# Performance work log

Measured on AMD Instinct MI355X. Metric: run time of the kernel, lower is better.

Reference implementation:

```python
import jax, jax.numpy as jnp
import numpy as np

B, C, H, W = 8, 64, 96, 320
K = 50
HEAD = 256
CLS = 3
CIN3 = C + 2 + CLS  # feat + 2 coord maps + one-hot class


def _conv(x, w, b, pad):
    y = jax.lax.conv_general_dilated(x, w, (1, 1), [(pad, pad), (pad, pad)],
                                     dimension_numbers=('NCHW', 'OIHW', 'NCHW'))
    return y + b[None, :, None, None]


def _head2(x, w1, b1, w2, b2):
    # Conv3x3 -> ReLU -> Conv1x1 (heatmap / offset_2d / size_2d heads)
    return _conv(jax.nn.relu(_conv(x, w1, b1, 1)), w2, b2, 0)


def _head3(x, w1, b1, g, be, m, v, w2, b2):
    # Conv3x3 -> BN(eval) -> ReLU -> AdaptiveAvgPool2d(1) -> Conv1x1, returns [N, cout]
    y = _conv(x, w1, b1, 1)
    y = (y - m[None, :, None, None]) * (g * jax.lax.rsqrt(v + 1e-5))[None, :, None, None] + be[None, :, None, None]
    y = jax.nn.relu(y).mean((2, 3))
    return y @ w2.reshape(w2.shape[0], -1).T + b2


def _nms(heat):
    hmax = jax.lax.reduce_window(heat, -jnp.inf, jax.lax.max, (1, 1, 3, 3), (1, 1, 1, 1), 'SAME')
    return jnp.where(hmax == heat, heat, 0.0)


def _roi_align(feat, boxes, out=7, sr=2):
    # torchvision roi_align semantics (spatial_scale=1, aligned=False, sampling_ratio=2);
    # boxes are treated as constants w.r.t. gradients (as in torchvision).
    boxes = jax.lax.stop_gradient(boxes)
    b = boxes[:, 0].astype(jnp.int32)
    x1, y1, x2, y2 = boxes[:, 1], boxes[:, 2], boxes[:, 3], boxes[:, 4]
    bw = jnp.maximum(x2 - x1, 1.0) / out
    bh = jnp.maximum(y2 - y1, 1.0) / out
    g = (jnp.arange(out * sr, dtype=feat.dtype) + 0.5) / sr  # sample positions in bin units
    ys = y1[:, None] + g[None, :] * bh[:, None]  # [N, S]
    xs = x1[:, None] + g[None, :] * bw[:, None]
    Hf, Wf = feat.shape[2], feat.shape[3]
    def prep(c, dim):
        valid = (c >= -1.0) & (c <= dim)
        c = jnp.clip(c, 0.0, dim - 1.0)
        i0 = jnp.floor(c).astype(jnp.int32)
        i1 = jnp.minimum(i0 + 1, dim - 1)
        return i0, i1, c - i0, valid
    y0, y1i, fy, vy = prep(ys, Hf)
    x0, x1i, fx, vx = prep(xs, Wf)
    bb = b[:, None, None]
    def gather(yi, xi):
        return feat[bb, :, yi[:, :, None], xi[:, None, :]]  # [N, S, S, C]
    w00 = ((1 - fy)[:, :, None] * (1 - fx)[:, None, :])[..., None]
    w01 = ((1 - fy)[:, :, None] * fx[:, None, :])[..., None]
    w10 = (fy[:, :, None] * (1 - fx)[:, None, :])[..., None]
    w11 = (fy[:, :, None] * fx[:, None, :])[..., None]
    val = gather(y0, x0) * w00 + gather(y0, x1i) * w01 + gather(y1i, x0) * w10 + gather(y1i, x1i) * w11
    val = val * (vy[:, :, None] & vx[:, None, :])[..., None].astype(feat.dtype)
    N = boxes.shape[0]
    val = val.reshape(N, out, sr, out, sr, -1).mean((2, 4))  # avg over sampling grid
    return val.transpose(0, 3, 1, 2)  # [N, C, 7, 7]


def _project2rect(calib, p):
    f_u, f_v = calib[:, 0, 0], calib[:, 1, 1]
    c_u, c_v = calib[:, 0, 2], calib[:, 1, 2]
    b_x = calib[:, 0, 3] / -f_u
    b_y = calib[:, 1, 3] / -f_v
    x = (p[:, 0] - c_u) * p[:, 2] / f_u + b_x
    y = (p[:, 1] - c_v) * p[:, 2] / f_v + b_y
    return jnp.stack([x, y, p[:, 2]], -1)


def reference(feat, coord_ranges, calibs, mean_size, hm_w1, hm_b1, hm_w2, hm_b2, o2_w1, o2_b1, o2_w2, o2_b2, s2_w1, s2_b1, s2_w2, s2_b2, dep_w1, dep_b1, dep_g, dep_be, dep_m, dep_v, dep_w2, dep_b2, o3_w1, o3_b1, o3_g, o3_be, o3_m, o3_v, o3_w2, o3_b2, s3_w1, s3_b1, s3_g, s3_be, s3_m, s3_v, s3_w2, s3_b2, hd_w1, hd_b1, hd_g, hd_be, hd_m, hd_v, hd_w2, hd_b2):
    # dense 2D heads
    heatmap = _head2(feat, hm_w1, hm_b1, hm_w2, hm_b2)        # [B,1,H,W]
    offset_2d = _head2(feat, o2_w1, o2_b1, o2_w2, o2_b2)      # [B,2,H,W]
    size_2d = _head2(feat, s2_w1, s2_b1, s2_w2, s2_b2)        # [B,2,H,W]
    # test-mode: NMS + topK (single-class heatmap -> cls ids all 0)
    heat = _nms(jnp.clip(jax.nn.sigmoid(heatmap), 1e-4, 1.0 - 1e-4))
    _, inds = jax.lax.top_k(heat.reshape(B, -1), K)           # [B,K]
    cls_flat = jnp.zeros((B * K,), jnp.int32)
    # box2d maps in feature coords
    xg = jnp.arange(W, dtype=feat.dtype)
    yg = jnp.arange(H, dtype=feat.dtype)
    coord_map = jnp.stack([jnp.broadcast_to(xg[None, :], (H, W)), jnp.broadcast_to(yg[:, None], (H, W))], 0)
    centre = coord_map[None] + offset_2d
    box2d = jnp.concatenate([centre - size_2d / 2, centre + size_2d / 2], 1)  # [B,4,H,W]
    bidx = jnp.broadcast_to(jnp.arange(B, dtype=feat.dtype)[:, None, None, None], (B, 1, H, W))
    bm = jnp.concatenate([bidx, box2d], 1).reshape(B, 5, H * W)
    boxes = jnp.take_along_axis(bm, inds[:, None, :], 2).transpose(0, 2, 1).reshape(B * K, 5)
    roi = _roi_align(feat, boxes)                             # [N,64,7,7]
    bsel = boxes[:, 0].astype(jnp.int32)
    cr = coord_ranges[bsel]
    sx = cr[:, 1, 0] - cr[:, 0, 0]
    sy = cr[:, 1, 1] - cr[:, 0, 1]
    boxes_r = jnp.stack([boxes[:, 0],
                         boxes[:, 1] / W * sx + cr[:, 0, 0],
                         boxes[:, 2] / H * sy + cr[:, 0, 1],
                         boxes[:, 3] / W * sx + cr[:, 0, 0],
                         boxes[:, 4] / H * sy + cr[:, 0, 1]], -1)
    roi_calibs = calibs[bsel]
    ones = jnp.ones((B * K, 1), feat.dtype)
    p1 = _project2rect(roi_calibs, jnp.concatenate([boxes_r[:, 1:3], ones], -1))[:, :2]
    p2 = _project2rect(roi_calibs, jnp.concatenate([boxes_r[:, 3:5], ones], -1))[:, :2]
    cam = jnp.concatenate([p1, p2], -1)                       # [N,4]
    t = jnp.arange(7, dtype=feat.dtype) / 6.0
    xs7 = cam[:, 0:1] + t[None, :] * (cam[:, 2:3] - cam[:, 0:1])
    ys7 = cam[:, 1:2] + t[None, :] * (cam[:, 3:4] - cam[:, 1:2])
    cmx = jnp.broadcast_to(xs7[:, None, None, :], (B * K, 1, 7, 7))
    cmy = jnp.broadcast_to(ys7[:, None, :, None], (B * K, 1, 7, 7))
    hots = jax.nn.one_hot(cls_flat, CLS, dtype=feat.dtype)
    roi_full = jnp.concatenate([roi, cmx, cmy, jnp.broadcast_to(hots[:, :, None, None], (B * K, CLS, 7, 7))], 1)
    h2d = jnp.maximum(boxes_r[:, 4] - boxes_r[:, 2], 1.0)
    s3 = _head3(roi_full, s3_w1, s3_b1, s3_g, s3_be, s3_m, s3_v, s3_w2, s3_b2)  # [N,4]
    h3d_log_std = s3[:, 3:4]
    size3d_offset = s3[:, :3]
    size_3d = mean_size[cls_flat] + size3d_offset
    f_u = roi_calibs[:, 0, 0]
    depth_geo = size_3d[:, 0] / h2d * f_u
    dno = _head3(roi_full, dep_w1, dep_b1, dep_g, dep_be, dep_m, dep_v, dep_w2, dep_b2)  # [N,2]
    geo_log_std = (h3d_log_std[:, 0] + 2.0 * (jnp.log(f_u) - jnp.log(h2d)))[:, None]
    net_log_std = jax.nn.logsumexp(jnp.concatenate([dno[:, 1:2], geo_log_std], -1), -1, keepdims=True)
    depth = jnp.concatenate([1.0 / (jax.nn.sigmoid(dno[:, 0:1]) + 1e-6) - 1.0 + depth_geo[:, None], net_log_std], -1)
    heading = _head3(roi_full, hd_w1, hd_b1, hd_g, hd_be, hd_m, hd_v, hd_w2, hd_b2)
    offset_3d = _head3(roi_full, o3_w1, o3_b1, o3_g, o3_be, o3_m, o3_v, o3_w2, o3_b2)
    return (heatmap, offset_2d, size_2d, heading, depth, offset_3d, size3d_offset, h3d_log_std)


def setup_inputs() -> dict:
    keys = iter(jax.random.split(jax.random.key(0), 40))
    def rn(shape, s=0.05):
        return jax.random.normal(next(keys), shape, jnp.float32) * s
    d = {}
    d['feat'] = jax.random.normal(next(keys), (B, C, H, W), jnp.float32)
    d['coord_ranges'] = jnp.tile(jnp.array([[0.0, 0.0], [1280.0, 384.0]], jnp.float32)[None], (B, 1, 1))
    d['calibs'] = jnp.tile(jnp.array([[720.0, 0.0, 640.0, 0.04], [0.0, 720.0, 190.0, 0.01], [0.0, 0.0, 1.0, 0.003]], jnp.float32)[None], (B, 1, 1))
    d['mean_size'] = jnp.array([[1.52, 1.63, 3.88], [1.73, 0.67, 0.88], [1.77, 0.60, 1.76]], jnp.float32)
    for pfx, cout in [('hm', 1), ('o2', 2), ('s2', 2)]:
        d[pfx + '_w1'] = rn((HEAD, C, 3, 3))
        d[pfx + '_b1'] = jnp.zeros((HEAD,), jnp.float32)
        d[pfx + '_w2'] = rn((cout, HEAD, 1, 1))
        d[pfx + '_b2'] = jnp.full((cout,), -2.19, jnp.float32) if pfx == 'hm' else jnp.zeros((cout,), jnp.float32)
    for pfx, cout in [('dep', 2), ('o3', 2), ('s3', 4), ('hd', 24)]:
        d[pfx + '_w1'] = rn((HEAD, CIN3, 3, 3))
        d[pfx + '_b1'] = jnp.zeros((HEAD,), jnp.float32)
        d[pfx + '_g'] = jnp.ones((HEAD,), jnp.float32)
        d[pfx + '_be'] = jnp.zeros((HEAD,), jnp.float32)
        d[pfx + '_m'] = jnp.zeros((HEAD,), jnp.float32)
        d[pfx + '_v'] = jnp.ones((HEAD,), jnp.float32)
        d[pfx + '_w2'] = rn((cout, HEAD, 1, 1))
        d[pfx + '_b2'] = jnp.zeros((cout,), jnp.float32)
    return d
```

## Files before the change

### kernel.cpp

```cpp
#include <hip/hip_runtime.h>


constexpr int OFF_O2    = 245760;
constexpr int OFF_S2    = 737280;
constexpr int OFF_HEAD  = 1228800;
constexpr int OFF_DEPTH = 1238400;
constexpr int OFF_O3D   = 1239200;
constexpr int OFF_S3D   = 1240000;
constexpr int OFF_H3D   = 1241200;

constexpr int WS_W1T  = 0;
constexpr int WS_BNSC = 635904;
constexpr int WS_BNSH = 636928;
constexpr int WS_KEEP = 637952;
constexpr int WS_INDS = 883712;
constexpr int WS_BOX  = 884112;
constexpr int WS_XS7  = 885712;
constexpr int WS_YS7  = 888512;
constexpr int WS_FU   = 891312;
constexpr int WS_H2D  = 891712;
constexpr int WS_DNO  = 892112;
constexpr int WS_ROIF = 892912;
constexpr int WS_SIG  = WS_ROIF;
constexpr int WS_W1R  = 2245312;
constexpr int WS_WPACK2 = 2245312;
constexpr int WS_FEATH  = 2540224;
constexpr int WS_FEATL  = 10618560;
constexpr long long FAST_REQ_BYTES = 18696896LL * 4;
constexpr int WS_WPACK3 = 18696896;
constexpr int WS_A3     = 19139264;
constexpr long long FAST3_REQ_BYTES = 20694464LL * 4;

typedef __attribute__((ext_vector_type(4))) float f32x4;
typedef __attribute__((ext_vector_type(8))) _Float16 f16x8;
typedef __attribute__((ext_vector_type(4))) unsigned int u32x4;

__global__ void repack_kernel(
    const float* __restrict__ w2h, const float* __restrict__ w2o, const float* __restrict__ w2s,
    const float* __restrict__ w3d, const float* __restrict__ w3o, const float* __restrict__ w3s, const float* __restrict__ w3h,
    const float* __restrict__ g0, const float* __restrict__ be0, const float* __restrict__ m0, const float* __restrict__ v0,
    const float* __restrict__ g1, const float* __restrict__ be1, const float* __restrict__ m1, const float* __restrict__ v1,
    const float* __restrict__ g2, const float* __restrict__ be2, const float* __restrict__ m2, const float* __restrict__ v2,
    const float* __restrict__ g3, const float* __restrict__ be3, const float* __restrict__ m3, const float* __restrict__ v3,
    float* __restrict__ ws)
{
  int i = blockIdx.x * 256 + threadIdx.x;
  if (i < 3 * 147456) {
    int br = i / 147456, r = i - br * 147456, q = r >> 8, c = r & 255;
    const float* src = br == 0 ? w2h : (br == 1 ? w2o : w2s);
    ws[WS_W1R + i] = src[c * 576 + q];
  } else if (i < 3 * 147456 + 4 * 158976) {
    int j = i - 3 * 147456;
    int br = j / 158976, r = j - br * 158976, q = r >> 8, c = r & 255;
    const float* src = br == 0 ? w3d : (br == 1 ? w3o : (br == 2 ? w3s : w3h));
    ws[WS_W1T + j] = src[c * 621 + q];
  } else {
    int j = i - (3 * 147456 + 4 * 158976);
    if (j < 1024) {
      int br = j >> 8, c = j & 255;
      const float* g  = br == 0 ? g0  : (br == 1 ? g1  : (br == 2 ? g2  : g3));
      const float* be = br == 0 ? be0 : (br == 1 ? be1 : (br == 2 ? be2 : be3));
      const float* m  = br == 0 ? m0  : (br == 1 ? m1  : (br == 2 ? m2  : m3));
      const float* v  = br == 0 ? v0  : (br == 1 ? v1  : (br == 2 ? v2  : v3));
      float sc = g[c] * rsqrtf(v[c] + 1e-5f);
      ws[WS_BNSC + j] = sc;
      ws[WS_BNSH + j] = be[c] - m[c] * sc;
    }
  }
}

__global__ void wpack2_kernel(const float* __restrict__ hm_w1, const float* __restrict__ o2_w1,
                              const float* __restrict__ s2_w1, float* __restrict__ ws)
{
  int i = blockIdx.x * 256 + threadIdx.x;
  if (i >= 4 * 18 * 256 * 32) return;
  int br = i / 147456; int r = i - br * 147456;
  int c = r / 8192; int r2 = r - c * 8192;
  int n = r2 >> 5; int kk = r2 & 31;
  int kg = c * 32 + kk;
  int tap = kg >> 6, ci = kg & 63;
  const float* w1 = (br == 0) ? o2_w1 : (br == 1 ? s2_w1 : hm_w1);
  float v = w1[n * 576 + ci * 9 + tap];
  _Float16 hi = (_Float16)v;
  _Float16 valh;
  if (br == 3) valh = (_Float16)(v - (float)hi);
  else valh = hi;
  unsigned short bits = __builtin_bit_cast(unsigned short, valh);
  long long didx = (((((long long)br * 18 + c) * 16 + (n >> 4)) * 4 + (kk >> 3)) * 128) + (n & 15) * 8 + (kk & 7);
  unsigned short* dst = (unsigned short*)(ws + WS_WPACK2);
  dst[didx] = bits;
}

__global__ void wpack3_kernel(const float* __restrict__ w3d, const float* __restrict__ w3o,
                              const float* __restrict__ w3s, const float* __restrict__ w3h,
                              float* __restrict__ ws)
{
  int i = blockIdx.x * 256 + threadIdx.x;
  if (i >= 4 * 27 * 256 * 32) return;
  int br = i / 221184; int r = i - br * 221184;
  int s = r / 8192; int r2 = r - s * 8192;
  int n = r2 >> 5; int kk = r2 & 31;
  int tap = s / 3; int cc = s - tap * 3;
  int ch = cc * 32 + kk;
  const float* w1 = br == 0 ? w3d : (br == 1 ? w3o : (br == 2 ? w3s : w3h));
  float v = (ch < 69) ? w1[n * 621 + ch * 9 + tap] : 0.f;
  unsigned short bits = __builtin_bit_cast(unsigned short, (_Float16)v);
  long long didx = (((((long long)br * 27 + s) * 16 + (n >> 4)) * 4 + (kk >> 3)) * 128) + (n & 15) * 8 + (kk & 7);
  ((unsigned short*)(ws + WS_WPACK3))[didx] = bits;
}

__global__ void pad_zero_kernel(float* __restrict__ ws)
{
  int i = blockIdx.x * 256 + threadIdx.x;
  if (i >= 428032) return;
  int arr = i / 214016; int r = i - arr * 214016;
  int px = r >> 5, q = r & 31;
  int b = px / 836, pr = px - b * 836;
  int yy, xx;
  if (pr < 322) { yy = 0; xx = pr; }
  else if (pr < 644) { yy = 97; xx = pr - 322; }
  else { int t = pr - 644; yy = 1 + (t >> 1); xx = (t & 1) * 321; }
  unsigned int* dst = (unsigned int*)(ws + (arr ? WS_FEATL : WS_FEATH));
  dst[((b * 98 + yy) * 322 + xx) * 32 + q] = 0u;
}

__global__ __launch_bounds__(256) void transpose_kernel(const float* __restrict__ feat, float* __restrict__ ws)
{
  __shared__ unsigned short T2[2][64 * 65];
  int bx = blockIdx.x;
  int b = bx / 480; int r = bx % 480; int y = r / 5; int x0 = (r % 5) * 64;
  int tid = threadIdx.x;
  int lx = tid & 63, grp = tid >> 6;
  #pragma unroll
  for (int it = 0; it < 16; ++it) {
    int ci = it * 4 + grp;
    float v = feat[(((b * 64 + ci) * 96 + y) * 320) + x0 + lx];
    _Float16 h = (_Float16)v;
    _Float16 l = (_Float16)(v - (float)h);
    T2[0][lx * 65 + ci] = __builtin_bit_cast(unsigned short, h);
    T2[1][lx * 65 + ci] = __builtin_bit_cast(unsigned short, l);
  }
  __syncthreads();
  unsigned int* fH = (unsigned int*)(ws + WS_FEATH);
  unsigned int* fL = (unsigned int*)(ws + WS_FEATL);
  #pragma unroll
  for (int it = 0; it < 16; ++it) {
    int unit = it * 256 + tid;
    int arr = unit >> 11; int un = unit & 2047;
    int x = un >> 5, pr = un & 31;
    unsigned int lo = T2[arr][x * 65 + pr * 2];
    unsigned int hi = T2[arr][x * 65 + pr * 2 + 1];
    unsigned int val = lo | (hi << 16);
    unsigned int* dst = arr ? fL : fH;
    dst[((b * 98 + y + 1) * 322 + (x0 + x + 1)) * 32 + pr] = val;
  }
}

__device__ __forceinline__ int tile_off(int row, int x, int j) {
  return ((row * 66 + x) * 8 + (j ^ (x & 7))) * 16;
}

__global__ __launch_bounds__(256, 2) void head2_os_kernel(
    const float* __restrict__ ws,
    const float* __restrict__ b1o, const float* __restrict__ b1s,
    const float* __restrict__ w2o, const float* __restrict__ w2s,
    const float* __restrict__ b2o, const float* __restrict__ b2s,
    float* __restrict__ out)
{
  __shared__ unsigned short tileH[4 * 66 * 64];
  __shared__ float red[1024];
  const int tid = threadIdx.x;
  const int l = tid & 63, w = tid >> 6;
  const int bx = blockIdx.x;
  const int b = bx / 240; int r = bx % 240;
  const int y0 = (r / 5) * 2; const int x0 = (r % 5) * 64;
  const unsigned short* fH = (const unsigned short*)(ws + WS_FEATH) + (size_t)b * (98 * 322 * 64);
  const _Float16* wpk = (const _Float16*)(ws + WS_WPACK2);

  for (int t = 0; t < 9; ++t) {
    int u = t * 256 + tid;
    if (u < 2112) {
      int row = u / 528; int rem = u - row * 528;
      int x = rem >> 3, j0 = rem & 7;
      u32x4 v = *(const u32x4*)(fH + ((y0 + row) * 322 + (x0 + x)) * 64 + j0 * 8);
      *(u32x4*)((char*)tileH + tile_off(row, x, j0)) = v;
    }
  }
  __syncthreads();

  const int l15 = l & 15, lg = l >> 4;

  #pragma unroll 1
  for (int br = 0; br < 2; ++br) {
    f32x4 acc[8][4];
    #pragma unroll
    for (int i = 0; i < 8; ++i)
      #pragma unroll
      for (int j = 0; j < 4; ++j) acc[i][j] = (f32x4)(0.f);

    f16x8 A0[8], A1[8], B0[4], B1[4];

    auto ldA = [&](f16x8* dst, int s) {
      int tap = s >> 1, half = s & 1;
      int ky = tap / 3, kx = tap - ky * 3;
      #pragma unroll
      for (int pf = 0; pf < 8; ++pf) {
        int p = pf * 16 + l15;
        int rr = p >> 6, xx = p & 63;
        dst[pf] = *(const f16x8*)((const char*)tileH + tile_off(rr + ky, xx + kx, half * 4 + lg));
      }
    };
    auto ldB = [&](f16x8* dst, int s) {
      #pragma unroll
      for (int nf = 0; nf < 4; ++nf)
        dst[nf] = *(const f16x8*)(wpk + ((((long long)br * 18 + s) * 16 + (w * 4 + nf)) * 4 + lg) * 128 + l15 * 8);
    };
    auto mm = [&](f16x8* A, f16x8* B) {
      #pragma unroll
      for (int pf = 0; pf < 8; ++pf)
        #pragma unroll
        for (int nf = 0; nf < 4; ++nf)
          acc[pf][nf] = __builtin_amdgcn_mfma_f32_16x16x32_f16(A[pf], B[nf], acc[pf][nf], 0, 0, 0);
    };

    ldA(A0, 0); ldB(B0, 0);
    #pragma unroll 1
    for (int s2 = 0; s2 < 9; ++s2) {
      const int s = s2 * 2;
      ldA(A1, s + 1); ldB(B1, s + 1);
      mm(A0, B0);
      if (s2 < 8) { ldA(A0, s + 2); ldB(B0, s + 2); }
      mm(A1, B1);
    }

    const float* b1 = br == 0 ? b1o : b1s;
    const float* w2 = br == 0 ? w2o : w2s;
    const float* b2 = br == 0 ? b2o : b2s;
    float b1v_[4], w2v[2][4];
    #pragma unroll
    for (int nf = 0; nf < 4; ++nf) {
      int n = w * 64 + nf * 16 + l15;
      b1v_[nf] = b1[n];
      w2v[0][nf] = w2[n];
      w2v[1][nf] = w2[256 + n];
    }
    __syncthreads();
    #pragma unroll
    for (int pf = 0; pf < 8; ++pf) {
      #pragma unroll
      for (int rr = 0; rr < 4; ++rr) {
        float s0 = 0.f, s1 = 0.f;
        #pragma unroll
        for (int nf = 0; nf < 4; ++nf) {
          float yv = acc[pf][nf][rr] + b1v_[nf];
          yv = yv > 0.f ? yv : 0.f;
          s0 = fmaf(w2v[0][nf], yv, s0);
          s1 = fmaf(w2v[1][nf], yv, s1);
        }
        #pragma unroll
        for (int m = 1; m < 16; m <<= 1) {
          s0 += __shfl_xor(s0, m);
          s1 += __shfl_xor(s1, m);
        }
        if (l15 == 0) {
          int p = pf * 16 + lg * 4 + rr;
          red[(w * 2 + 0) * 128 + p] = s0;
          red[(w * 2 + 1) * 128 + p] = s1;
        }
      }
    }
    __syncthreads();
    {
      int p = tid & 127, o = tid >> 7;
      float s = red[(0 * 2 + o) * 128 + p] + red[(1 * 2 + o) * 128 + p] +
                red[(2 * 2 + o) * 128 + p] + red[(3 * 2 + o) * 128 + p] + b2[o];
      int ypix = y0 + (p >> 6), xpix = x0 + (p & 63);
      int base = (br == 0) ? OFF_O2 : OFF_S2;
      out[base + ((b * 2 + o) * 96 + ypix) * 320 + xpix] = s;
    }
  }
}

__global__ __launch_bounds__(256, 2) void head2_hm_kernel(
    const float* __restrict__ ws,
    const float* __restrict__ b1h, const float* __restrict__ w2h, const float* __restrict__ b2h,
    float* __restrict__ out)
{
  __shared__ unsigned short tiles[2][3 * 66 * 64];
  __shared__ float red[256];
  const int tid = threadIdx.x;
  const int l = tid & 63, w = tid >> 6;
  const int bx = blockIdx.x;
  const int b = bx / 480; int r = bx % 480;
  const int y = r / 5; const int x0 = (r % 5) * 64;
  const unsigned short* fH = (const unsigned short*)(ws + WS_FEATH) + (size_t)b * (98 * 322 * 64);
  const unsigned short* fL = (const unsigned short*)(ws + WS_FEATL) + (size_t)b * (98 * 322 * 64);
  const _Float16* wpk = (const _Float16*)(ws + WS_WPACK2);

  for (int t = 0; t < 13; ++t) {
    int u = t * 256 + tid;
    if (u < 3168) {
      int arr = u >= 1584; int uu = u - arr * 1584;
      int row = uu / 528; int rem = uu - row * 528;
      int x = rem >> 3, j0 = rem & 7;
      const unsigned short* src = arr ? fL : fH;
      u32x4 v = *(const u32x4*)(src + ((y + row) * 322 + (x0 + x)) * 64 + j0 * 8);
      *(u32x4*)((char*)&tiles[arr][0] + tile_off(row, x, j0)) = v;
    }
  }
  __syncthreads();

  const int l15 = l & 15, lg = l >> 4;

  f32x4 acc[4][4];
  #pragma unroll
  for (int i = 0; i < 4; ++i)
    #pragma unroll
    for (int j = 0; j < 4; ++j) acc[i][j] = (f32x4)(0.f);

  f16x8 AH0[4], AL0[4], AH1[4], AL1[4];
  f16x8 BH0[4], BL0[4], BH1[4], BL1[4];

  auto ldA = [&](f16x8* ah, f16x8* al, int s) {
    int tap = s >> 1, half = s & 1;
    int ky = tap / 3, kx = tap - ky * 3;
    #pragma unroll
    for (int pf = 0; pf < 4; ++pf) {
      int p = pf * 16 + l15;
      int off = tile_off(ky, p + kx, half * 4 + lg);
      ah[pf] = *(const f16x8*)((const char*)&tiles[0][0] + off);
      al[pf] = *(const f16x8*)((const char*)&tiles[1][0] + off);
    }
  };
  auto ldB = [&](f16x8* bh, f16x8* bl, int s) {
    #pragma unroll
    for (int nf = 0; nf < 4; ++nf) {
      bh[nf] = *(const f16x8*)(wpk + (((2LL * 18 + s) * 16 + (w * 4 + nf)) * 4 + lg) * 128 + l15 * 8);
      bl[nf] = *(const f16x8*)(wpk + (((3LL * 18 + s) * 16 + (w * 4 + nf)) * 4 + lg) * 128 + l15 * 8);
    }
  };
  auto mm3 = [&](f16x8* ah, f16x8* al, f16x8* bh, f16x8* bl) {
    #pragma unroll
    for (int pf = 0; pf < 4; ++pf)
      #pragma unroll
      for (int nf = 0; nf < 4; ++nf)
        acc[pf][nf] = __builtin_amdgcn_mfma_f32_16x16x32_f16(ah[pf], bh[nf], acc[pf][nf], 0, 0, 0);
    #pragma unroll
    for (int pf = 0; pf < 4; ++pf)
      #pragma unroll
      for (int nf = 0; nf < 4; ++nf)
        acc[pf][nf] = __builtin_amdgcn_mfma_f32_16x16x32_f16(ah[pf], bl[nf], acc[pf][nf], 0, 0, 0);
    #pragma unroll
    for (int pf = 0; pf < 4; ++pf)
      #pragma unroll
      for (int nf = 0; nf < 4; ++nf)
        acc[pf][nf] = __builtin_amdgcn_mfma_f32_16x16x32_f16(al[pf], bh[nf], acc[pf][nf], 0, 0, 0);
  };

  ldA(AH0, AL0, 0); ldB(BH0, BL0, 0);
  #pragma unroll 1
  for (int s2 = 0; s2 < 9; ++s2) {
    const int s = s2 * 2;
    ldA(AH1, AL1, s + 1); ldB(BH1, BL1, s + 1);
    mm3(AH0, AL0, BH0, BL0);
    if (s2 < 8) { ldA(AH0, AL0, s + 2); ldB(BH0, BL0, s + 2); }
    mm3(AH1, AL1, BH1, BL1);
  }

  float b1v_[4], w2v[4];
  #pragma unroll
  for (int nf = 0; nf < 4; ++nf) {
    int n = w * 64 + nf * 16 + l15;
    b1v_[nf] = b1h[n];
    w2v[nf] = w2h[n];
  }
  __syncthreads();
  #pragma unroll
  for (int pf = 0; pf < 4; ++pf) {
    #pragma unroll
    for (int rr = 0; rr < 4; ++rr) {
      float s0 = 0.f;
      #pragma unroll
      for (int nf = 0; nf < 4; ++nf) {
        float yv = acc[pf][nf][rr] + b1v_[nf];
        yv = yv > 0.f ? yv : 0.f;
        s0 = fmaf(w2v[nf], yv, s0);
      }
      #pragma unroll
      for (int m = 1; m < 16; m <<= 1) s0 += __shfl_xor(s0, m);
      if (l15 == 0) red[w * 64 + pf * 16 + lg * 4 + rr] = s0;
    }
  }
  __syncthreads();
  if (tid < 64) {
    float s = red[tid] + red[64 + tid] + red[128 + tid] + red[192 + tid] + b2h[0];
    out[(b * 96 + y) * 320 + x0 + tid] = s;
  }
}

__global__ __launch_bounds__(256) void head2_kernel(
    const float* __restrict__ feat, const float* __restrict__ ws,
    const float* __restrict__ b1h, const float* __restrict__ b1o, const float* __restrict__ b1s,
    const float* __restrict__ w2h, const float* __restrict__ w2o, const float* __restrict__ w2s,
    const float* __restrict__ b2h, const float* __restrict__ b2o, const float* __restrict__ b2s,
    float* __restrict__ out)
{
  __shared__ float xs[32 * 10 * 34];
  const int tid = threadIdx.x;
  const int tx = tid & 31, ty = tid >> 5;
  const int x0 = blockIdx.x * 32, y0 = blockIdx.y * 8, bz = blockIdx.z;
  const int px = x0 + tx, py = y0 + ty;
  const float* w1r = ws + WS_W1R;

  #pragma unroll 1
  for (int br = 0; br < 3; ++br) {
    const float* wr = w1r + br * 147456;
    const float* b1 = br == 0 ? b1h : (br == 1 ? b1o : b1s);
    const float* w2 = br == 0 ? w2h : (br == 1 ? w2o : w2s);
    const int cout = (br == 0) ? 1 : 2;
    float acc0 = 0.f, acc1 = 0.f;
    #pragma unroll 1
    for (int c0 = 0; c0 < 256; c0 += 64) {
      float part[64];
      #pragma unroll
      for (int j = 0; j < 64; ++j) part[j] = 0.f;
      #pragma unroll 1
      for (int cc = 0; cc < 2; ++cc) {
        for (int i = tid; i < 32 * 10 * 34; i += 256) {
          int ci = i / 340; int rr = i - ci * 340; int ry = rr / 34; int rx = rr - ry * 34;
          int gy = y0 + ry - 1, gx = x0 + rx - 1;
          float v = 0.f;
          if ((unsigned)gy < 96u && (unsigned)gx < 320u)
            v = feat[((bz * 64 + cc * 32 + ci) * 96 + gy) * 320 + gx];
          xs[i] = v;
        }
        __syncthreads();
        #pragma unroll 1
        for (int ci = 0; ci < 32; ++ci) {
          const float* wp = wr + ((cc * 32 + ci) * 9) * 256 + c0;
          const float* xb = &xs[ci * 340 + ty * 34 + tx];
          #pragma unroll
          for (int k = 0; k < 9; ++k) {
            float xv = xb[(k / 3) * 34 + (k % 3)];
            const float* wk = wp + k * 256;
            #pragma unroll
            for (int j = 0; j < 64; ++j) part[j] = fmaf(wk[j], xv, part[j]);
          }
        }
        __syncthreads();
// ... 142 lines not shown
  float bx2 = ws[WS_BOX + n * 4 + 2], by2 = ws[WS_BOX + n * 4 + 3];
  if (tid < 14) {
    float bh = fmaxf(by2 - by1, 1.f) / 7.f;
    float g = ((float)tid + 0.5f) * 0.5f;
    float c = by1 + g * bh;
    vy[tid] = (c >= -1.f && c <= 96.f) ? 1.f : 0.f;
    c = fminf(fmaxf(c, 0.f), 95.f);
    int i0 = (int)floorf(c);
    iy0[tid] = i0; iy1[tid] = (i0 + 1 < 95) ? i0 + 1 : 95;
    fy[tid] = c - (float)i0;
  } else if (tid < 28) {
    int t = tid - 14;
    float bw = fmaxf(bx2 - bx1, 1.f) / 7.f;
    float g = ((float)t + 0.5f) * 0.5f;
    float c = bx1 + g * bw;
    vx[t] = (c >= -1.f && c <= 320.f) ? 1.f : 0.f;
    c = fminf(fmaxf(c, 0.f), 319.f);
    int i0 = (int)floorf(c);
    ix0[t] = i0; ix1[t] = (i0 + 1 < 319) ? i0 + 1 : 319;
    fx[t] = c - (float)i0;
  }
  __syncthreads();
  int bsel = n / 50;
  const float* fbase = feat + bsel * 64 * 30720;
  float* rf = ws + WS_ROIF + n * 3381;
  for (int i = tid; i < 64 * 49; i += 256) {
    int c = i / 49, p = i - c * 49;
    int oy = p / 7, ox = p - oy * 7;
    const float* fb = fbase + c * 30720;
    float s = 0.f;
    #pragma unroll
    for (int sy2 = 0; sy2 < 2; ++sy2) {
      #pragma unroll
      for (int sx2 = 0; sx2 < 2; ++sx2) {
        int jy = oy * 2 + sy2, jx = ox * 2 + sx2;
        const float* r0 = fb + iy0[jy] * 320;
        const float* r1 = fb + iy1[jy] * 320;
        float gy = fy[jy], gx = fx[jx];
        float v00 = r0[ix0[jx]], v01 = r0[ix1[jx]], v10 = r1[ix0[jx]], v11 = r1[ix1[jx]];
        float v = v00 * (1.f - gy) * (1.f - gx) + v01 * (1.f - gy) * gx
                + v10 * gy * (1.f - gx) + v11 * gy * gx;
        s += v * vy[jy] * vx[jx];
      }
    }
    rf[c * 49 + p] = s * 0.25f;
  }
  if (tid < 5 * 49) {
    int ch = tid / 49, p = tid - ch * 49;
    int oy = p / 7, ox = p - oy * 7;
    float v;
    if (ch == 0) v = ws[WS_XS7 + n * 7 + ox];
    else if (ch == 1) v = ws[WS_YS7 + n * 7 + oy];
    else if (ch == 2) v = 1.f;
    else v = 0.f;
    rf[(64 + ch) * 49 + p] = v;
  }
}

__global__ void roi16_kernel(float* __restrict__ ws)
{
  int n = blockIdx.x;
  const float* rf = ws + WS_ROIF + n * 3381;
  unsigned short* a3 = (unsigned short*)(ws + WS_A3) + (size_t)n * 7776;
  for (int t = 0; t < 31; ++t) {
    int i = t * 256 + threadIdx.x;
    if (i < 7776) {
      int pr = i / 96, ch = i - pr * 96;
      int py = pr / 9, px = pr - py * 9;
      float v = 0.f;
      if (py >= 1 && py <= 7 && px >= 1 && px <= 7 && ch < 69)
        v = rf[ch * 49 + (py - 1) * 7 + (px - 1)];
      a3[i] = __builtin_bit_cast(unsigned short, (_Float16)v);
    }
  }
}

__global__ __launch_bounds__(256, 2) void head3m_kernel(
    float* __restrict__ ws,
    const float* __restrict__ b1d, const float* __restrict__ b1o3, const float* __restrict__ b1s3, const float* __restrict__ b1hd,
    const float* __restrict__ w2d, const float* __restrict__ w2o3, const float* __restrict__ w2s3, const float* __restrict__ w2hd,
    const float* __restrict__ b2d, const float* __restrict__ b2o3, const float* __restrict__ b2s3, const float* __restrict__ b2hd,
    float* __restrict__ out)
{
  __shared__ unsigned short A[81 * 104];
  __shared__ float ym[256];
  const int tid = threadIdx.x;
  const int l = tid & 63, w = tid >> 6;
  const int l15 = l & 15, lg = l >> 4;
  const int n = blockIdx.x;
  const unsigned short* a3 = (const unsigned short*)(ws + WS_A3) + (size_t)n * 7776;
  const _Float16* wp3 = (const _Float16*)(ws + WS_WPACK3);

  #pragma unroll
  for (int t = 0; t < 4; ++t) {
    int u = t * 256 + tid;
    if (u < 972) {
      int row = u / 12, cu = u - row * 12;
      u32x4 v = *(const u32x4*)(a3 + u * 8);
      *(u32x4*)((char*)A + (row * 104 + cu * 8) * 2) = v;
    }
  }
  __syncthreads();

  int rbase[4];
  #pragma unroll
  for (int pf = 0; pf < 4; ++pf) {
    int p = pf * 16 + l15;
    rbase[pf] = (p < 49) ? ((p / 7) * 9 + (p % 7)) : 0;
  }

  #pragma unroll 1
  for (int br = 0; br < 4; ++br) {
    const float* b1 = br == 0 ? b1d : (br == 1 ? b1o3 : (br == 2 ? b1s3 : b1hd));
    const float* w2 = br == 0 ? w2d : (br == 1 ? w2o3 : (br == 2 ? w2s3 : w2hd));
    const float* b2 = br == 0 ? b2d : (br == 1 ? b2o3 : (br == 2 ? b2s3 : b2hd));
    const int cout = br == 0 ? 2 : (br == 1 ? 2 : (br == 2 ? 4 : 24));

    f32x4 acc[4][4];
    #pragma unroll
    for (int i = 0; i < 4; ++i)
      #pragma unroll
      for (int j = 0; j < 4; ++j) acc[i][j] = (f32x4)(0.f);

    f16x8 A0[4], A1[4], B0[4], B1[4];

    auto ldA = [&](f16x8* dst, int s) {
      int tap = s / 3, cc = s - tap * 3;
      int ky = tap / 3, kx = tap - ky * 3;
      #pragma unroll
      for (int pf = 0; pf < 4; ++pf) {
        int rr = rbase[pf] + ky * 9 + kx;
        dst[pf] = *(const f16x8*)((const char*)A + (rr * 104 + cc * 32 + lg * 8) * 2);
      }
    };
    auto ldB = [&](f16x8* dst, int s) {
      #pragma unroll
      for (int nf = 0; nf < 4; ++nf)
        dst[nf] = *(const f16x8*)(wp3 + ((((long long)br * 27 + s) * 16 + (w * 4 + nf)) * 4 + lg) * 128 + l15 * 8);
    };
    auto mm = [&](f16x8* Af, f16x8* Bf) {
      #pragma unroll
      for (int pf = 0; pf < 4; ++pf)
        #pragma unroll
        for (int nf = 0; nf < 4; ++nf)
          acc[pf][nf] = __builtin_amdgcn_mfma_f32_16x16x32_f16(Af[pf], Bf[nf], acc[pf][nf], 0, 0, 0);
    };

    ldA(A0, 0); ldB(B0, 0);
    #pragma unroll 1
    for (int s2 = 0; s2 < 13; ++s2) {
      const int s = s2 * 2;
      ldA(A1, s + 1); ldB(B1, s + 1);
      mm(A0, B0);
      ldA(A0, s + 2); ldB(B0, s + 2);
      mm(A1, B1);
    }
    mm(A0, B0);

    #pragma unroll
    for (int nf = 0; nf < 4; ++nf) {
      int nn = w * 64 + nf * 16 + l15;
      float b1n = b1[nn];
      float scn = ws[WS_BNSC + br * 256 + nn];
      float shn = ws[WS_BNSH + br * 256 + nn];
      float local = 0.f;
      #pragma unroll
      for (int pf = 0; pf < 4; ++pf) {
        #pragma unroll
        for (int rr = 0; rr < 4; ++rr) {
          int p = pf * 16 + lg * 4 + rr;
          float yv = (acc[pf][nf][rr] + b1n) * scn + shn;
          yv = yv > 0.f ? yv : 0.f;
          local += (p < 49) ? yv : 0.f;
        }
      }
      local += __shfl_xor(local, 16);
      local += __shfl_xor(local, 32);
      if (lg == 0) ym[nn] = local;
    }
    __syncthreads();
    for (int o = w; o < cout; o += 4) {
      float p = 0.f;
      #pragma unroll
      for (int t = 0; t < 4; ++t) p = fmaf(w2[o * 256 + t * 64 + l], ym[t * 64 + l], p);
      p *= (1.f / 49.f);
      #pragma unroll
      for (int off = 32; off > 0; off >>= 1) p += __shfl_down(p, off);
      if (l == 0) {
        float v = p + b2[o];
        if (br == 0) ws[WS_DNO + n * 2 + o] = v;
        else if (br == 1) out[OFF_O3D + n * 2 + o] = v;
        else if (br == 2) { if (o < 3) out[OFF_S3D + n * 3 + o] = v; else out[OFF_H3D + n] = v; }
        else out[OFF_HEAD + n * 24 + o] = v;
      }
    }
    __syncthreads();
  }
}

__global__ __launch_bounds__(256) void head3_kernel(
    float* ws,
    const float* __restrict__ b1d, const float* __restrict__ b1o3, const float* __restrict__ b1s3, const float* __restrict__ b1hd,
    const float* __restrict__ w2d, const float* __restrict__ w2o3, const float* __restrict__ w2s3, const float* __restrict__ w2hd,
    const float* __restrict__ b2d, const float* __restrict__ b2o3, const float* __restrict__ b2s3, const float* __restrict__ b2hd,
    float* __restrict__ out)
{
  int n = blockIdx.x, br = blockIdx.y;
  int c = threadIdx.x;
  __shared__ float ym[256];
  const float* wt = ws + WS_W1T + br * 158976;
  const float* b1 = br == 0 ? b1d : (br == 1 ? b1o3 : (br == 2 ? b1s3 : b1hd));
  const float* w2 = br == 0 ? w2d : (br == 1 ? w2o3 : (br == 2 ? w2s3 : w2hd));
  const float* b2 = br == 0 ? b2d : (br == 1 ? b2o3 : (br == 2 ? b2s3 : b2hd));
  const int cout = br == 0 ? 2 : (br == 1 ? 2 : (br == 2 ? 4 : 24));
  const float* xin0 = ws + WS_ROIF + n * 3381;

  float acc[49];
  #pragma unroll
  for (int i = 0; i < 49; ++i) acc[i] = 0.f;

  #pragma unroll 1
  for (int ci = 0; ci < 69; ++ci) {
    float wv[9];
    #pragma unroll
    for (int k = 0; k < 9; ++k) wv[k] = wt[(ci * 9 + k) * 256 + c];
    const float* xin = xin0 + ci * 49;
    #pragma unroll
    for (int y = 0; y < 7; ++y) {
      float xr[9];
      xr[0] = 0.f; xr[8] = 0.f;
      #pragma unroll
      for (int q = 0; q < 7; ++q) xr[q + 1] = xin[y * 7 + q];
      #pragma unroll
      for (int ky = 0; ky < 3; ++ky) {
        int pyy = y + 1 - ky;
        if (pyy >= 0 && pyy < 7) {
          #pragma unroll
          for (int kx = 0; kx < 3; ++kx) {
            float w = wv[ky * 3 + kx];
            #pragma unroll
// ... 31 lines not shown
    }
  }
}

__global__ void depth_kernel(const float* ws, const float* __restrict__ mean_size, float* __restrict__ out)
{
  int n = blockIdx.x * 256 + threadIdx.x;
  if (n >= 400) return;
  float h3d = out[OFF_H3D + n];
  float s30 = out[OFF_S3D + n * 3];
  float size0 = mean_size[0] + s30;
  float f = ws[WS_FU + n], h = ws[WS_H2D + n];
  float dgeo = size0 / h * f;
  float geo = h3d + 2.f * (logf(f) - logf(h));
  float a = ws[WS_DNO + n * 2 + 1];
  float mx = fmaxf(a, geo);
  float nls = mx + logf(expf(a - mx) + expf(geo - mx));
  float sg = 1.f / (1.f + expf(-ws[WS_DNO + n * 2]));
  out[OFF_DEPTH + n * 2] = 1.f / (sg + 1e-6f) - 1.f + dgeo;
  out[OFF_DEPTH + n * 2 + 1] = nls;
}

extern "C" void kernel_launch(void* const* d_in, const int* in_sizes, int n_in,
                              void* d_out, int out_size, void* d_ws, size_t ws_size,
                              hipStream_t stream)
{
  const float* feat         = (const float*)d_in[0];
  const float* coord_ranges = (const float*)d_in[1];
  const float* calibs       = (const float*)d_in[2];
  const float* mean_size    = (const float*)d_in[3];
  const float* hm_w1 = (const float*)d_in[4];
  const float* hm_b1 = (const float*)d_in[5];
  const float* hm_w2 = (const float*)d_in[6];
  const float* hm_b2 = (const float*)d_in[7];
  const float* o2_w1 = (const float*)d_in[8];
  const float* o2_b1 = (const float*)d_in[9];
  const float* o2_w2 = (const float*)d_in[10];
  const float* o2_b2 = (const float*)d_in[11];
  const float* s2_w1 = (const float*)d_in[12];
  const float* s2_b1 = (const float*)d_in[13];
  const float* s2_w2 = (const float*)d_in[14];
  const float* s2_b2 = (const float*)d_in[15];
  const float* dep_w1 = (const float*)d_in[16];
  const float* dep_b1 = (const float*)d_in[17];
  const float* dep_g  = (const float*)d_in[18];
  const float* dep_be = (const float*)d_in[19];
  const float* dep_m  = (const float*)d_in[20];
  const float* dep_v  = (const float*)d_in[21];
  const float* dep_w2 = (const float*)d_in[22];
  const float* dep_b2 = (const float*)d_in[23];
  const float* o3_w1 = (const float*)d_in[24];
  const float* o3_b1 = (const float*)d_in[25];
  const float* o3_g  = (const float*)d_in[26];
  const float* o3_be = (const float*)d_in[27];
  const float* o3_m  = (const float*)d_in[28];
  const float* o3_v  = (const float*)d_in[29];
  const float* o3_w2 = (const float*)d_in[30];
  const float* o3_b2 = (const float*)d_in[31];
  const float* s3_w1 = (const float*)d_in[32];
  const float* s3_b1 = (const float*)d_in[33];
  const float* s3_g  = (const float*)d_in[34];
  const float* s3_be = (const float*)d_in[35];
  const float* s3_m  = (const float*)d_in[36];
  const float* s3_v  = (const float*)d_in[37];
  const float* s3_w2 = (const float*)d_in[38];
  const float* s3_b2 = (const float*)d_in[39];
  const float* hd_w1 = (const float*)d_in[40];
  const float* hd_b1 = (const float*)d_in[41];
  const float* hd_g  = (const float*)d_in[42];
  const float* hd_be = (const float*)d_in[43];
  const float* hd_m  = (const float*)d_in[44];
  const float* hd_v  = (const float*)d_in[45];
  const float* hd_w2 = (const float*)d_in[46];
  const float* hd_b2 = (const float*)d_in[47];

  float* out = (float*)d_out;
  float* ws  = (float*)d_ws;
  bool fast  = (long long)ws_size >= FAST_REQ_BYTES;
  bool fast3 = (long long)ws_size >= FAST3_REQ_BYTES;

  repack_kernel<<<dim3((3 * 147456 + 4 * 158976 + 1024 + 255) / 256), 256, 0, stream>>>(
      hm_w1, o2_w1, s2_w1, dep_w1, o3_w1, s3_w1, hd_w1,
      dep_g, dep_be, dep_m, dep_v, o3_g, o3_be, o3_m, o3_v,
      s3_g, s3_be, s3_m, s3_v, hd_g, hd_be, hd_m, hd_v, ws);

  if (fast) {
    wpack2_kernel<<<dim3((4 * 18 * 256 * 32 + 255) / 256), 256, 0, stream>>>(hm_w1, o2_w1, s2_w1, ws);
    pad_zero_kernel<<<dim3((428032 + 255) / 256), 256, 0, stream>>>(ws);
    transpose_kernel<<<dim3(3840), 256, 0, stream>>>(feat, ws);
    head2_os_kernel<<<dim3(1920), 256, 0, stream>>>(ws, o2_b1, s2_b1, o2_w2, s2_w2, o2_b2, s2_b2, out);
    head2_hm_kernel<<<dim3(3840), 256, 0, stream>>>(ws, hm_b1, hm_w2, hm_b2, out);
  } else {
    head2_kernel<<<dim3(10, 12, 8), 256, 0, stream>>>(feat, ws,
        hm_b1, o2_b1, s2_b1, hm_w2, o2_w2, s2_w2, hm_b2, o2_b2, s2_b2, out);
  }
  if (fast3)
    wpack3_kernel<<<dim3((4 * 27 * 256 * 32 + 255) / 256), 256, 0, stream>>>(dep_w1, o3_w1, s3_w1, hd_w1, ws);

  nms_sig_kernel<<<dim3(960), 256, 0, stream>>>(out, ws + WS_SIG);
  nms_max_kernel<<<dim3(960), 256, 0, stream>>>(ws + WS_SIG, ws + WS_KEEP);
  topk_kernel<<<dim3(8), 256, 0, stream>>>(ws);
  boxes_kernel<<<dim3(2), 256, 0, stream>>>(out, coord_ranges, calibs, ws);
  roi_kernel<<<dim3(400), 256, 0, stream>>>(feat, ws);
  if (fast3) {
    roi16_kernel<<<dim3(400), 256, 0, stream>>>(ws);
    head3m_kernel<<<dim3(400), 256, 0, stream>>>(ws,
        dep_b1, o3_b1, s3_b1, hd_b1, dep_w2, o3_w2, s3_w2, hd_w2,
        dep_b2, o3_b2, s3_b2, hd_b2, out);
  } else {
    head3_kernel<<<dim3(400, 4), 256, 0, stream>>>(ws,
        dep_b1, o3_b1, s3_b1, hd_b1, dep_w2, o3_w2, s3_w2, hd_w2,
        dep_b2, o3_b2, s3_b2, hd_b2, out);
  }
  depth_kernel<<<dim3(2), 256, 0, stream>>>(ws, mean_size, out);
}
```

Measured before the change: 588.2 us.

## Re-layout LDS tiles, fully unroll MFMA loops, skip unused fp32 weight repacks

```diff
diff --git a/kernel.cpp b/kernel.cpp
--- a/kernel.cpp
+++ b/kernel.cpp
@@ -42,14 +42,16 @@
     const float* __restrict__ g1, const float* __restrict__ be1, const float* __restrict__ m1, const float* __restrict__ v1,
     const float* __restrict__ g2, const float* __restrict__ be2, const float* __restrict__ m2, const float* __restrict__ v2,
     const float* __restrict__ g3, const float* __restrict__ be3, const float* __restrict__ m3, const float* __restrict__ v3,
-    float* __restrict__ ws)
+    int skip2, int skip3, float* __restrict__ ws)
 {
   int i = blockIdx.x * 256 + threadIdx.x;
   if (i < 3 * 147456) {
+    if (skip2) return;
     int br = i / 147456, r = i - br * 147456, q = r >> 8, c = r & 255;
     const float* src = br == 0 ? w2h : (br == 1 ? w2o : w2s);
     ws[WS_W1R + i] = src[c * 576 + q];
   } else if (i < 3 * 147456 + 4 * 158976) {
+    if (skip3) return;
     int j = i - 3 * 147456;
     int br = j / 158976, r = j - br * 158976, q = r >> 8, c = r & 255;
     const float* src = br == 0 ? w3d : (br == 1 ? w3o : (br == 2 ? w3s : w3h));
@@ -156,18 +158,15 @@
   }
 }
 
-__device__ __forceinline__ int tile_off(int row, int x, int j) {
-  return ((row * 66 + x) * 8 + (j ^ (x & 7))) * 16;
-}
-
-__global__ __launch_bounds__(256, 2) void head2_os_kernel(
+
+__global__ __launch_bounds__(256, 3) void head2_os_kernel(
     const float* __restrict__ ws,
     const float* __restrict__ b1o, const float* __restrict__ b1s,
     const float* __restrict__ w2o, const float* __restrict__ w2s,
     const float* __restrict__ b2o, const float* __restrict__ b2s,
     float* __restrict__ out)
 {
-  __shared__ unsigned short tileH[4 * 66 * 64];
+  __shared__ unsigned char tile[4 * 8 * 66 * 16];
   __shared__ float red[1024];
   const int tid = threadIdx.x;
   const int l = tid & 63, w = tid >> 6;
@@ -183,12 +182,13 @@
       int row = u / 528; int rem = u - row * 528;
       int x = rem >> 3, j0 = rem & 7;
       u32x4 v = *(const u32x4*)(fH + ((y0 + row) * 322 + (x0 + x)) * 64 + j0 * 8);
-      *(u32x4*)((char*)tileH + tile_off(row, x, j0)) = v;
+      *(u32x4*)(tile + ((row * 8 + j0) * 66 + x) * 16) = v;
     }
   }
   __syncthreads();
 
   const int l15 = l & 15, lg = l >> 4;
+  const int aBase = (lg * 66 + l15) * 16;
 
   #pragma unroll 1
   for (int br = 0; br < 2; ++br) {
@@ -198,39 +198,27 @@
       #pragma unroll
       for (int j = 0; j < 4; ++j) acc[i][j] = (f32x4)(0.f);
 
-    f16x8 A0[8], A1[8], B0[4], B1[4];
-
-    auto ldA = [&](f16x8* dst, int s) {
-      int tap = s >> 1, half = s & 1;
-      int ky = tap / 3, kx = tap - ky * 3;
+    const _Float16* wB = wpk + (((long long)(br * 18) * 16 + w * 4) * 4 + lg) * 128 + l15 * 8;
+
+    #pragma unroll
+    for (int s = 0; s < 18; ++s) {
+      const int tap = s >> 1, half = s & 1;
+      const int ky = tap / 3, kx = tap - ky * 3;
+      const int stepOff = ((ky * 8 + half * 4) * 66 + kx) * 16;
+      f16x8 af[8], bf[4];
       #pragma unroll
       for (int pf = 0; pf < 8; ++pf) {
-        int p = pf * 16 + l15;
-        int rr = p >> 6, xx = p & 63;
-        dst[pf] = *(const f16x8*)((const char*)tileH + tile_off(rr + ky, xx + kx, half * 4 + lg));
+        const int frOff = (pf < 4) ? pf * 256 : 8448 + (pf - 4) * 256;
+        af[pf] = *(const f16x8*)(tile + aBase + frOff + stepOff);
       }
-    };
-    auto ldB = [&](f16x8* dst, int s) {
       #pragma unroll
       for (int nf = 0; nf < 4; ++nf)
-        dst[nf] = *(const f16x8*)(wpk + ((((long long)br * 18 + s) * 16 + (w * 4 + nf)) * 4 + lg) * 128 + l15 * 8);
-    };
-    auto mm = [&](f16x8* A, f16x8* B) {
+        bf[nf] = *(const f16x8*)(wB + s * 8192 + nf * 512);
       #pragma unroll
       for (int pf = 0; pf < 8; ++pf)
         #pragma unroll
         for (int nf = 0; nf < 4; ++nf)
-          acc[pf][nf] = __builtin_amdgcn_mfma_f32_16x16x32_f16(A[pf], B[nf], acc[pf][nf], 0, 0, 0);
-    };
-
-    ldA(A0, 0); ldB(B0, 0);
-    #pragma unroll 1
-    for (int s2 = 0; s2 < 9; ++s2) {
-      const int s = s2 * 2;
-      ldA(A1, s + 1); ldB(B1, s + 1);
-      mm(A0, B0);
-      if (s2 < 8) { ldA(A0, s + 2); ldB(B0, s + 2); }
-      mm(A1, B1);
+          acc[pf][nf] = __builtin_amdgcn_mfma_f32_16x16x32_f16(af[pf], bf[nf], acc[pf][nf], 0, 0, 0);
     }
 
     const float* b1 = br == 0 ? b1o : b1s;
@@ -281,12 +269,12 @@
   }
 }
 
-__global__ __launch_bounds__(256, 2) void head2_hm_kernel(
+__global__ __launch_bounds__(256, 3) void head2_hm_kernel(
     const float* __restrict__ ws,
     const float* __restrict__ b1h, const float* __restrict__ w2h, const float* __restrict__ b2h,
     float* __restrict__ out)
 {
-  __shared__ unsigned short tiles[2][3 * 66 * 64];
+  __shared__ unsigned char tiles[2 * 3 * 8 * 66 * 16];
   __shared__ float red[256];
   const int tid = threadIdx.x;
   const int l = tid & 63, w = tid >> 6;
@@ -305,12 +293,13 @@
       int x = rem >> 3, j0 = rem & 7;
       const unsigned short* src = arr ? fL : fH;
       u32x4 v = *(const u32x4*)(src + ((y + row) * 322 + (x0 + x)) * 64 + j0 * 8);
-      *(u32x4*)((char*)&tiles[arr][0] + tile_off(row, x, j0)) = v;
+      *(u32x4*)(tiles + arr * 25344 + ((row * 8 + j0) * 66 + x) * 16) = v;
     }
   }
   __syncthreads();
 
   const int l15 = l & 15, lg = l >> 4;
+  const int aBase = (lg * 66 + l15) * 16;
 
   f32x4 acc[4][4];
   #pragma unroll
@@ -318,28 +307,25 @@
     #pragma unroll
     for (int j = 0; j < 4; ++j) acc[i][j] = (f32x4)(0.f);
 
-  f16x8 AH0[4], AL0[4], AH1[4], AL1[4];
-  f16x8 BH0[4], BL0[4], BH1[4], BL1[4];
-
-  auto ldA = [&](f16x8* ah, f16x8* al, int s) {
-    int tap = s >> 1, half = s & 1;
-    int ky = tap / 3, kx = tap - ky * 3;
+  const _Float16* wBH = wpk + (((long long)(2 * 18) * 16 + w * 4) * 4 + lg) * 128 + l15 * 8;
+  const _Float16* wBL = wpk + (((long long)(3 * 18) * 16 + w * 4) * 4 + lg) * 128 + l15 * 8;
+
+  #pragma unroll
+  for (int s = 0; s < 18; ++s) {
+    const int tap = s >> 1, half = s & 1;
+    const int ky = tap / 3, kx = tap - ky * 3;
+    const int stepOff = ((ky * 8 + half * 4) * 66 + kx) * 16;
+    f16x8 ah[4], al[4], bh[4], bl[4];
     #pragma unroll
     for (int pf = 0; pf < 4; ++pf) {
-      int p = pf * 16 + l15;
-      int off = tile_off(ky, p + kx, half * 4 + lg);
-      ah[pf] = *(const f16x8*)((const char*)&tiles[0][0] + off);
-      al[pf] = *(const f16x8*)((const char*)&tiles[1][0] + off);
-    }
-  };
-  auto ldB = [&](f16x8* bh, f16x8* bl, int s) {
+      ah[pf] = *(const f16x8*)(tiles + aBase + pf * 256 + stepOff);
+      al[pf] = *(const f16x8*)(tiles + 25344 + aBase + pf * 256 + stepOff);
+    }
     #pragma unroll
     for (int nf = 0; nf < 4; ++nf) {
-      bh[nf] = *(const f16x8*)(wpk + (((2LL * 18 + s) * 16 + (w * 4 + nf)) * 4 + lg) * 128 + l15 * 8);
-      bl[nf] = *(const f16x8*)(wpk + (((3LL * 18 + s) * 16 + (w * 4 + nf)) * 4 + lg) * 128 + l15 * 8);
-    }
-  };
-  auto mm3 = [&](f16x8* ah, f16x8* al, f16x8* bh, f16x8* bl) {
+      bh[nf] = *(const f16x8*)(wBH + s * 8192 + nf * 512);
+      bl[nf] = *(const f16x8*)(wBL + s * 8192 + nf * 512);
+    }
     #pragma unroll
     for (int pf = 0; pf < 4; ++pf)
       #pragma unroll
@@ -355,16 +341,6 @@
       #pragma unroll
       for (int nf = 0; nf < 4; ++nf)
         acc[pf][nf] = __builtin_amdgcn_mfma_f32_16x16x32_f16(al[pf], bh[nf], acc[pf][nf], 0, 0, 0);
-  };
-
-  ldA(AH0, AL0, 0); ldB(BH0, BL0, 0);
-  #pragma unroll 1
-  for (int s2 = 0; s2 < 9; ++s2) {
-    const int s = s2 * 2;
-    ldA(AH1, AL1, s + 1); ldB(BH1, BL1, s + 1);
-    mm3(AH0, AL0, BH0, BL0);
-    if (s2 < 8) { ldA(AH0, AL0, s + 2); ldB(BH0, BL0, s + 2); }
-    mm3(AH1, AL1, BH1, BL1);
   }
 
   float b1v_[4], w2v[4];
@@ -673,7 +649,7 @@
     const float* __restrict__ b2d, const float* __restrict__ b2o3, const float* __restrict__ b2s3, const float* __restrict__ b2hd,
     float* __restrict__ out)
 {
-  __shared__ unsigned short A[81 * 104];
+  __shared__ unsigned char A[81 * 104 * 2];
   __shared__ float ym[256];
   const int tid = threadIdx.x;
   const int l = tid & 63, w = tid >> 6;
@@ -688,16 +664,17 @@
     if (u < 972) {
       int row = u / 12, cu = u - row * 12;
       u32x4 v = *(const u32x4*)(a3 + u * 8);
-      *(u32x4*)((char*)A + (row * 104 + cu * 8) * 2) = v;
+      *(u32x4*)(A + (row * 104 + cu * 8) * 2) = v;
     }
   }
   __syncthreads();
 
-  int rbase[4];
+  int aB[4];
   #pragma unroll
   for (int pf = 0; pf < 4; ++pf) {
     int p = pf * 16 + l15;
-    rbase[pf] = (p < 49) ? ((p / 7) * 9 + (p % 7)) : 0;
+    int rb = (p < 49) ? ((p / 7) * 9 + (p % 7)) : 0;
+    aB[pf] = rb * 208 + lg * 16;
   }
 
   #pragma unroll 1
@@ -713,40 +690,26 @@
       #pragma unroll
       for (int j = 0; j < 4; ++j) acc[i][j] = (f32x4)(0.f);
 
-    f16x8 A0[4], A1[4], B0[4], B1[4];
-
-    auto ldA = [&](f16x8* dst, int s) {
-      int tap = s / 3, cc = s - tap * 3;
-      int ky = tap / 3, kx = tap - ky * 3;
-      #pragma unroll
-      for (int pf = 0; pf < 4; ++pf) {
-        int rr = rbase[pf] + ky * 9 + kx;
-        dst[pf] = *(const f16x8*)((const char*)A + (rr * 104 + cc * 32 + lg * 8) * 2);
-      }
-    };
-    auto ldB = [&](f16x8* dst, int s) {
+    const _Float16* wB3 = wp3 + (((long long)(br * 27) * 16 + w * 4) * 4 + lg) * 128 + l15 * 8;
+
+    #pragma unroll
+    for (int s = 0; s < 27; ++s) {
+      const int tap = s / 3, cc = s - tap * 3;
+      const int ky = tap / 3, kx = tap - ky * 3;
+      const int stepOff = (ky * 9 + kx) * 208 + cc * 64;
+      f16x8 af[4], bf[4];
+      #pragma unroll
+      for (int pf = 0; pf < 4; ++pf)
+        af[pf] = *(const f16x8*)(A + aB[pf] + stepOff);
       #pragma unroll
       for (int nf = 0; nf < 4; ++nf)
-        dst[nf] = *(const f16x8*)(wp3 + ((((long long)br * 27 + s) * 16 + (w * 4 + nf)) * 4 + lg) * 128 + l15 * 8);
-    };
-    auto mm = [&](f16x8* Af, f16x8* Bf) {
+        bf[nf] = *(const f16x8*)(wB3 + s * 8192 + nf * 512);
       #pragma unroll
       for (int pf = 0; pf < 4; ++pf)
         #pragma unroll
         for (int nf = 0; nf < 4; ++nf)
-          acc[pf][nf] = __builtin_amdgcn_mfma_f32_16x16x32_f16(Af[pf], Bf[nf], acc[pf][nf], 0, 0, 0);
-    };
-
-    ldA(A0, 0); ldB(B0, 0);
-    #pragma unroll 1
-    for (int s2 = 0; s2 < 13; ++s2) {
-      const int s = s2 * 2;
-      ldA(A1, s + 1); ldB(B1, s + 1);
-      mm(A0, B0);
-      ldA(A0, s + 2); ldB(B0, s + 2);
-      mm(A1, B1);
-    }
-    mm(A0, B0);
+          acc[pf][nf] = __builtin_amdgcn_mfma_f32_16x16x32_f16(af[pf], bf[nf], acc[pf][nf], 0, 0, 0);
+    }
 
     #pragma unroll
     for (int nf = 0; nf < 4; ++nf) {
@@ -944,7 +907,8 @@
   repack_kernel<<<dim3((3 * 147456 + 4 * 158976 + 1024 + 255) / 256), 256, 0, stream>>>(
       hm_w1, o2_w1, s2_w1, dep_w1, o3_w1, s3_w1, hd_w1,
       dep_g, dep_be, dep_m, dep_v, o3_g, o3_be, o3_m, o3_v,
-      s3_g, s3_be, s3_m, s3_v, hd_g, hd_be, hd_m, hd_v, ws);
+      s3_g, s3_be, s3_m, s3_v, hd_g, hd_be, hd_m, hd_v,
+      fast ? 1 : 0, fast3 ? 1 : 0, ws);
 
   if (fast) {
     wpack2_kernel<<<dim3((4 * 18 * 256 * 32 + 255) / 256), 256, 0, stream>>>(hm_w1, o2_w1, s2_w1, ws);
```

Measured after the change: 1.023 ms. +74.0%, slower.
